# Optimization experiments

Measured on AMD Instinct MI355X. Metric: run time of the kernel, lower is better.

Reference implementation:

```python
import jax, jax.numpy as jnp
import numpy as np

D_MODEL = 1024
MAX_BIRTHS = 4
BIRTH_THRESHOLD = 0.45


def setup_inputs() -> dict:
    key = jax.random.key(0)
    ks = jax.random.split(key, 5)
    B, Tu, Tm, D = 4, 4096, 2048, D_MODEL
    return {
        "o_micro": jax.random.normal(ks[0], (B, Tu, D), jnp.float32),
        "o_macro": jax.random.normal(ks[1], (B, Tm, D), jnp.float32),
        "r_emer_acc": jax.random.uniform(ks[2], (B, Tu, Tm), jnp.float32),
        "chunk_size": 128,
        # vesica_field: Linear(2D -> D, no bias); torch weight layout (D, 2D)
        "W_vesica": jax.random.normal(ks[3], (D, 2 * D), jnp.float32) * (1.0 / np.sqrt(2.0 * D)),
        # birth_gate: Linear(D -> 1)
        "w_gate": jax.random.normal(ks[4], (D,), jnp.float32) * (1.0 / np.sqrt(float(D))),
        "b_gate": jnp.zeros((), jnp.float32),
        "threshold_bias": jnp.zeros((), jnp.float32),
    }


def reference(o_micro, o_macro, r_emer_acc, chunk_size, W_vesica, w_gate, b_gate, threshold_bias):
    B, Tu, D = o_micro.shape
    # accumulated resonance per micro token: mean over macro dim -> (B, Tu)
    micro_res = r_emer_acc.mean(axis=-1)
    # adjacent-pair resonance -> (B, Tu-1)
    pair_res = (micro_res[:, :-1] + micro_res[:, 1:]) * 0.5
    threshold = BIRTH_THRESHOLD + jnp.tanh(threshold_bias) * 0.2
    above = pair_res > threshold
    pair_scores = pair_res * above.astype(pair_res.dtype)
    k = MAX_BIRTHS  # min(max_births, Tu-1); Tu >> max_births here
    topk_vals, topk_idx = jax.lax.top_k(pair_scores, k)  # (B, k)
    birth_mask = topk_vals > 0
    n_births = birth_mask.sum()
    # gather parent pairs -> (B, k, D) each
    left = jnp.take_along_axis(o_micro, topk_idx[..., None], axis=1)
    right = jnp.take_along_axis(o_micro, (topk_idx + 1)[..., None], axis=1)
    combined = jnp.concatenate([left, right], axis=-1)  # (B, k, 2D)
    child = jnp.einsum("bkf,df->bkd", combined, W_vesica)
    gate = jax.nn.sigmoid(jnp.einsum("bkd,d->bk", child, w_gate) + b_gate)
    child = child * gate[..., None] * birth_mask[..., None].astype(child.dtype)
    # compact born children to the front (stable), zeros pad the tail —
    # identical to the torch ragged stack+pad given fixed width k
    order = jnp.argsort(~birth_mask, axis=1, stable=True)  # (B, k)
    child = jnp.take_along_axis(child, order[..., None], axis=1)
    o_macro_expanded = jnp.concatenate([o_macro, child], axis=1)  # (B, Tm+k, D)
    return o_macro_expanded, n_births
```

## Files before the change

### kernel.cpp

```cpp
#include <hip/hip_runtime.h>
#include <math.h>

#define BATCH 4
#define TU 4096
#define TM 2048
#define DM 1024
#define FF 2048
#define KB 4
#define NROWS (BATCH*KB)
#define OUT_TM (TM+KB)

__global__ __launch_bounds__(256) void k_mean_copy(
    const float* __restrict__ r_emer, const float* __restrict__ o_macro,
    float* __restrict__ micro_res, float* __restrict__ out)
{
    const int tid  = threadIdx.x;
    const int lane = tid & 63;
    const int wave = tid >> 6;
    const int row  = blockIdx.x * 4 + wave;

    const float4* rp = (const float4*)(r_emer + (size_t)row * FF);
    float s = 0.0f;
    #pragma unroll
    for (int j = 0; j < 8; ++j) {
        float4 v = rp[lane + 64 * j];
        s += v.x + v.y + v.z + v.w;
    }
    #pragma unroll
    for (int off = 32; off >= 1; off >>= 1)
        s += __shfl_down(s, off, 64);
    if (lane == 0) micro_res[row] = s * (1.0f / 2048.0f);

    const float4* src = (const float4*)o_macro;
    float4* dst = (float4*)out;
    const int NF4       = BATCH * TM * DM / 4;
    const int PER_BATCH = TM * DM / 4;
    const int DST_BATCH = OUT_TM * DM / 4;
    for (int e = blockIdx.x * 256 + tid; e < NF4; e += gridDim.x * 256) {
        int b = e >> 19;
        int q = e & (PER_BATCH - 1);
        dst[b * DST_BATCH + q] = src[e];
    }
}

__global__ __launch_bounds__(256) void k_topk(
    const float* __restrict__ micro_res,
    const float* __restrict__ threshold_bias,
    int* __restrict__ topk_idx, float* __restrict__ topk_val)
{
    __shared__ float res[TU];
    __shared__ float rv[256];
    __shared__ int   ri[256];
    __shared__ int   sel[KB];
    __shared__ float selv[KB];

    const int b = blockIdx.x, tid = threadIdx.x;
    const float* mr = micro_res + b * TU;
    for (int i = tid; i < TU; i += 256) res[i] = mr[i];
    __syncthreads();

    const float thr = 0.45f + tanhf(threshold_bias[0]) * 0.2f;

    for (int p = 0; p < KB; ++p) {
        float bv = -1.0f; int bi = 0x7fffffff;
        for (int t = tid; t < TU - 1; t += 256) {
            bool skip = false;
            for (int q = 0; q < p; ++q) if (sel[q] == t) skip = true;
            if (skip) continue;
            float pr = (res[t] + res[t + 1]) * 0.5f;
            float sc = pr > thr ? pr : 0.0f;
            if (sc > bv || (sc == bv && t < bi)) { bv = sc; bi = t; }
        }
        rv[tid] = bv; ri[tid] = bi;
        __syncthreads();
        for (int s = 128; s >= 1; s >>= 1) {
            if (tid < s) {
                float ov = rv[tid + s]; int oi = ri[tid + s];
                if (ov > rv[tid] || (ov == rv[tid] && oi < ri[tid])) {
                    rv[tid] = ov; ri[tid] = oi;
                }
            }
            __syncthreads();
        }
        if (tid == 0) { sel[p] = ri[0]; selv[p] = rv[0]; }
        __syncthreads();
    }
    if (tid < KB) {
        topk_idx[b * KB + tid] = sel[tid];
        topk_val[b * KB + tid] = selv[tid];
    }
}

__global__ __launch_bounds__(256) void k_child(
    const float* __restrict__ o_micro, const float* __restrict__ W,
    const int* __restrict__ topk_idx, float* __restrict__ child_raw)
{
    const int d   = blockIdx.x;
    const int tid = threadIdx.x;
    const int lane = tid & 63;
    const int wave = tid >> 6;
    const int f0  = tid * 8;

    __shared__ int sidx[NROWS];
    if (tid < NROWS) sidx[tid] = topk_idx[tid];
    __syncthreads();

    const float4* wp = (const float4*)(W + (size_t)d * FF + f0);
    const float4 w0 = wp[0], w1 = wp[1];

    float acc[NROWS];
    #pragma unroll
    for (int r = 0; r < NROWS; ++r) {
        const int bb  = r >> 2;
        const int idx = sidx[r];
        const float* srcrow;
        int fo;
        if (f0 < DM) { srcrow = o_micro + ((size_t)bb * TU + idx) * DM;     fo = f0; }
        else         { srcrow = o_micro + ((size_t)bb * TU + idx + 1) * DM; fo = f0 - DM; }
        const float4* cp = (const float4*)(srcrow + fo);
        float4 c0 = cp[0], c1 = cp[1];
        acc[r] = c0.x * w0.x + c0.y * w0.y + c0.z * w0.z + c0.w * w0.w
               + c1.x * w1.x + c1.y * w1.y + c1.z * w1.z + c1.w * w1.w;
    }

    #pragma unroll
    for (int r = 0; r < NROWS; ++r) {
        float v = acc[r];
        #pragma unroll
        for (int off = 32; off >= 1; off >>= 1)
            v += __shfl_down(v, off, 64);
        acc[r] = v;
    }
    __shared__ float part[4][NROWS];
    if (lane == 0) {
        #pragma unroll
        for (int r = 0; r < NROWS; ++r) part[wave][r] = acc[r];
    }
    __syncthreads();
    if (tid < NROWS)
        child_raw[(size_t)tid * DM + d] =
            part[0][tid] + part[1][tid] + part[2][tid] + part[3][tid];
}

__global__ __launch_bounds__(256) void k_gate(
    const float* __restrict__ child_raw, const float* __restrict__ w_gate,
    const float* __restrict__ b_gate, const float* __restrict__ topk_val,
    float* __restrict__ out)
{
    const int row = blockIdx.x;
    const int b = row >> 2, k = row & 3;
    const int tid = threadIdx.x;
    const int lane = tid & 63, wave = tid >> 6;

    const float4* cp = (const float4*)(child_raw + (size_t)row * DM);
    const float4* wp = (const float4*)w_gate;
    float4 c = cp[tid], w = wp[tid];
    float dotp = c.x * w.x + c.y * w.y + c.z * w.z + c.w * w.w;

    #pragma unroll
    for (int off = 32; off >= 1; off >>= 1)
        dotp += __shfl_down(dotp, off, 64);

    __shared__ float ps[4];
    __shared__ float scale_s;
    if (lane == 0) ps[wave] = dotp;
    __syncthreads();
    if (tid == 0) {
        float dsum = ps[0] + ps[1] + ps[2] + ps[3] + b_gate[0];
        float gate = 1.0f / (1.0f + expf(-dsum));
        float mask = topk_val[row] > 0.0f ? 1.0f : 0.0f;
        scale_s = gate * mask;
    }
    __syncthreads();

    const float s = scale_s;
    float4 o; o.x = c.x * s; o.y = c.y * s; o.z = c.z * s; o.w = c.w * s;
    float4* op = (float4*)(out + ((size_t)b * OUT_TM + TM + k) * DM);
    op[tid] = o;

    if (row == 0 && tid == 0) {
        int n = 0;
        for (int i = 0; i < NROWS; ++i) n += (topk_val[i] > 0.0f) ? 1 : 0;
        out[(size_t)BATCH * OUT_TM * DM] = (float)n;
    }
}

extern "C" void kernel_launch(void* const* d_in, const int* in_sizes, int n_in,
                              void* d_out, int out_size, void* d_ws, size_t ws_size,
                              hipStream_t stream) {
    const float* o_micro   = (const float*)d_in[0];
    const float* o_macro   = (const float*)d_in[1];
    const float* r_emer    = (const float*)d_in[2];
    const float* W_vesica  = (const float*)d_in[4];
    const float* w_gate    = (const float*)d_in[5];
    const float* b_gate    = (const float*)d_in[6];
    const float* thr_bias  = (const float*)d_in[7];
    float* out = (float*)d_out;

    float* wsf       = (float*)d_ws;
    float* micro_res = wsf;
    int*   topk_idx  = (int*)(wsf + 16384);
    float* topk_val  = wsf + 16400;
    float* child_raw = wsf + 16416;

    k_mean_copy<<<4096, 256, 0, stream>>>(r_emer, o_macro, micro_res, out);
    k_topk<<<BATCH, 256, 0, stream>>>(micro_res, thr_bias, topk_idx, topk_val);
    k_child<<<DM, 256, 0, stream>>>(o_micro, W_vesica, topk_idx, child_raw);
    k_gate<<<NROWS, 256, 0, stream>>>(child_raw, w_gate, b_gate, topk_val, out);
}
```

Before: 307.5 us.

## Precompute gate vector W^T·w_gate, fuse gate into topk, overlap macro copy with child GEMV

Uses associativity so the gate logit is computed as combined·(W^T w_gate). The vector u = W^T w_gate is built by extra blocks inside the mean kernel, and the topk kernel applies it right after selection. The child GEMV then writes scaled results straight into the output, and the o_macro copy moves into the same launch as the child blocks. This drops one kernel launch and the child_raw round trip. In exchange the topk kernel does more serial work and rounding order changes slightly.

```diff
diff --git a/kernel.cpp b/kernel.cpp
--- a/kernel.cpp
+++ b/kernel.cpp
@@ -10,56 +10,62 @@
 #define NROWS (BATCH*KB)
 #define OUT_TM (TM+KB)
 
-__global__ __launch_bounds__(256) void k_mean_copy(
-    const float* __restrict__ r_emer, const float* __restrict__ o_macro,
-    float* __restrict__ micro_res, float* __restrict__ out)
+__global__ __launch_bounds__(256) void k_mean_u(
+    const float* __restrict__ r_emer, const float* __restrict__ W,
+    const float* __restrict__ w_gate,
+    float* __restrict__ micro_res, float* __restrict__ partials)
 {
-    const int tid  = threadIdx.x;
-    const int lane = tid & 63;
-    const int wave = tid >> 6;
-    const int row  = blockIdx.x * 4 + wave;
-
-    const float4* rp = (const float4*)(r_emer + (size_t)row * FF);
-    float s = 0.0f;
-    #pragma unroll
-    for (int j = 0; j < 8; ++j) {
-        float4 v = rp[lane + 64 * j];
-        s += v.x + v.y + v.z + v.w;
-    }
-    #pragma unroll
-    for (int off = 32; off >= 1; off >>= 1)
-        s += __shfl_down(s, off, 64);
-    if (lane == 0) micro_res[row] = s * (1.0f / 2048.0f);
-
-    const float4* src = (const float4*)o_macro;
-    float4* dst = (float4*)out;
-    const int NF4       = BATCH * TM * DM / 4;
-    const int PER_BATCH = TM * DM / 4;
-    const int DST_BATCH = OUT_TM * DM / 4;
-    for (int e = blockIdx.x * 256 + tid; e < NF4; e += gridDim.x * 256) {
-        int b = e >> 19;
-        int q = e & (PER_BATCH - 1);
-        dst[b * DST_BATCH + q] = src[e];
-    }
-}
-
-__global__ __launch_bounds__(256) void k_topk(
-    const float* __restrict__ micro_res,
-    const float* __restrict__ threshold_bias,
-    int* __restrict__ topk_idx, float* __restrict__ topk_val)
+    const int tid = threadIdx.x;
+    const int blk = blockIdx.x;
+    if (blk < 4096) {
+        const int lane = tid & 63, wave = tid >> 6;
+        const int row = blk * 4 + wave;
+        const float4* rp = (const float4*)(r_emer + (size_t)row * FF);
+        float s = 0.0f;
+        #pragma unroll
+        for (int j = 0; j < 8; ++j) {
+            float4 v = rp[lane + 64 * j];
+            s += v.x + v.y + v.z + v.w;
+        }
+        #pragma unroll
+        for (int off = 32; off >= 1; off >>= 1)
+            s += __shfl_down(s, off, 64);
+        if (lane == 0) micro_res[row] = s * (1.0f / 2048.0f);
+    } else {
+        const int i  = blk - 4096;
+        const int di = i >> 3;
+        const int f  = (i & 7) * 256 + tid;
+        const int d0 = di * 128;
+        const float* wp = W + (size_t)d0 * FF + f;
+        float acc = 0.0f;
+        #pragma unroll 4
+        for (int d = 0; d < 128; ++d)
+            acc += w_gate[d0 + d] * wp[(size_t)d * FF];
+        partials[di * FF + f] = acc;
+    }
+}
+
+__global__ __launch_bounds__(256) void k_topk_gate(
+    const float* __restrict__ micro_res, const float* __restrict__ thr_bias,
+    const float* __restrict__ o_micro, const float* __restrict__ partials,
+    const float* __restrict__ b_gate,
+    int* __restrict__ sel_out, float* __restrict__ s_out,
+    float* __restrict__ cnt_out)
 {
     __shared__ float res[TU];
     __shared__ float rv[256];
     __shared__ int   ri[256];
     __shared__ int   sel[KB];
     __shared__ float selv[KB];
+    __shared__ float red[4];
 
     const int b = blockIdx.x, tid = threadIdx.x;
+    const int lane = tid & 63, wave = tid >> 6;
     const float* mr = micro_res + b * TU;
     for (int i = tid; i < TU; i += 256) res[i] = mr[i];
     __syncthreads();
 
-    const float thr = 0.45f + tanhf(threshold_bias[0]) * 0.2f;
+    const float thr = 0.45f + tanhf(thr_bias[0]) * 0.2f;
 
     for (int p = 0; p < KB; ++p) {
         float bv = -1.0f; int bi = 0x7fffffff;
@@ -85,103 +91,118 @@
         if (tid == 0) { sel[p] = ri[0]; selv[p] = rv[0]; }
         __syncthreads();
     }
-    if (tid < KB) {
-        topk_idx[b * KB + tid] = sel[tid];
-        topk_val[b * KB + tid] = selv[tid];
-    }
-}
-
-__global__ __launch_bounds__(256) void k_child(
+
+    float su[8];
+    #pragma unroll
+    for (int j = 0; j < 8; ++j) su[j] = 0.0f;
+    const float4* pp = (const float4*)partials;
+    #pragma unroll
+    for (int di = 0; di < 8; ++di) {
+        float4 p0 = pp[di * 512 + tid * 2];
+        float4 p1 = pp[di * 512 + tid * 2 + 1];
+        su[0] += p0.x; su[1] += p0.y; su[2] += p0.z; su[3] += p0.w;
+        su[4] += p1.x; su[5] += p1.y; su[6] += p1.z; su[7] += p1.w;
+    }
+
+    for (int k = 0; k < KB; ++k) {
+        const int idx = sel[k];
+        const float* rowp = (tid < 128)
+            ? o_micro + ((size_t)b * TU + idx) * DM + tid * 8
+            : o_micro + ((size_t)b * TU + idx + 1) * DM + (tid - 128) * 8;
+        float4 c0 = ((const float4*)rowp)[0];
+        float4 c1 = ((const float4*)rowp)[1];
+        float dp = c0.x*su[0] + c0.y*su[1] + c0.z*su[2] + c0.w*su[3]
+                 + c1.x*su[4] + c1.y*su[5] + c1.z*su[6] + c1.w*su[7];
+        #pragma unroll
+        for (int off = 32; off >= 1; off >>= 1)
+            dp += __shfl_down(dp, off, 64);
+        if (lane == 0) red[wave] = dp;
+        __syncthreads();
+        if (tid == 0) {
+            float dot  = red[0] + red[1] + red[2] + red[3] + b_gate[0];
+            float gate = 1.0f / (1.0f + expf(-dot));
+            float mask = selv[k] > 0.0f ? 1.0f : 0.0f;
+            s_out[b * KB + k]   = gate * mask;
+            sel_out[b * KB + k] = sel[k];
+        }
+        __syncthreads();
+    }
+    if (tid == 0) {
+        int c = 0;
+        #pragma unroll
+        for (int k = 0; k < KB; ++k) c += (selv[k] > 0.0f) ? 1 : 0;
+        cnt_out[b] = (float)c;
+    }
+}
+
+__global__ __launch_bounds__(256) void k_child_copy(
     const float* __restrict__ o_micro, const float* __restrict__ W,
-    const int* __restrict__ topk_idx, float* __restrict__ child_raw)
+    const float* __restrict__ o_macro,
+    const int* __restrict__ sel_in, const float* __restrict__ s_in,
+    const float* __restrict__ cnt_in, float* __restrict__ out)
 {
-    const int d   = blockIdx.x;
     const int tid = threadIdx.x;
-    const int lane = tid & 63;
-    const int wave = tid >> 6;
-    const int f0  = tid * 8;
-
-    __shared__ int sidx[NROWS];
-    if (tid < NROWS) sidx[tid] = topk_idx[tid];
-    __syncthreads();
-
-    const float4* wp = (const float4*)(W + (size_t)d * FF + f0);
-    const float4 w0 = wp[0], w1 = wp[1];
-
-    float acc[NROWS];
-    #pragma unroll
-    for (int r = 0; r < NROWS; ++r) {
-        const int bb  = r >> 2;
-        const int idx = sidx[r];
-        const float* srcrow;
-        int fo;
-        if (f0 < DM) { srcrow = o_micro + ((size_t)bb * TU + idx) * DM;     fo = f0; }
-        else         { srcrow = o_micro + ((size_t)bb * TU + idx + 1) * DM; fo = f0 - DM; }
-        const float4* cp = (const float4*)(srcrow + fo);
-        float4 c0 = cp[0], c1 = cp[1];
-        acc[r] = c0.x * w0.x + c0.y * w0.y + c0.z * w0.z + c0.w * w0.w
-               + c1.x * w1.x + c1.y * w1.y + c1.z * w1.z + c1.w * w1.w;
-    }
-
-    #pragma unroll
-    for (int r = 0; r < NROWS; ++r) {
-        float v = acc[r];
-        #pragma unroll
-        for (int off = 32; off >= 1; off >>= 1)
-            v += __shfl_down(v, off, 64);
-        acc[r] = v;
-    }
-    __shared__ float part[4][NROWS];
-    if (lane == 0) {
-        #pragma unroll
-        for (int r = 0; r < NROWS; ++r) part[wave][r] = acc[r];
-    }
-    __syncthreads();
-    if (tid < NROWS)
-        child_raw[(size_t)tid * DM + d] =
-            part[0][tid] + part[1][tid] + part[2][tid] + part[3][tid];
-}
-
-__global__ __launch_bounds__(256) void k_gate(
-    const float* __restrict__ child_raw, const float* __restrict__ w_gate,
-    const float* __restrict__ b_gate, const float* __restrict__ topk_val,
-    float* __restrict__ out)
-{
-    const int row = blockIdx.x;
-    const int b = row >> 2, k = row & 3;
-    const int tid = threadIdx.x;
-    const int lane = tid & 63, wave = tid >> 6;
-
-    const float4* cp = (const float4*)(child_raw + (size_t)row * DM);
-    const float4* wp = (const float4*)w_gate;
-    float4 c = cp[tid], w = wp[tid];
-    float dotp = c.x * w.x + c.y * w.y + c.z * w.z + c.w * w.w;
-
-    #pragma unroll
-    for (int off = 32; off >= 1; off >>= 1)
-        dotp += __shfl_down(dotp, off, 64);
-
-    __shared__ float ps[4];
-    __shared__ float scale_s;
-    if (lane == 0) ps[wave] = dotp;
-    __syncthreads();
-    if (tid == 0) {
-        float dsum = ps[0] + ps[1] + ps[2] + ps[3] + b_gate[0];
-        float gate = 1.0f / (1.0f + expf(-dsum));
-        float mask = topk_val[row] > 0.0f ? 1.0f : 0.0f;
-        scale_s = gate * mask;
-    }
-    __syncthreads();
-
-    const float s = scale_s;
-    float4 o; o.x = c.x * s; o.y = c.y * s; o.z = c.z * s; o.w = c.w * s;
-    float4* op = (float4*)(out + ((size_t)b * OUT_TM + TM + k) * DM);
-    op[tid] = o;
-
-    if (row == 0 && tid == 0) {
-        int n = 0;
-        for (int i = 0; i < NROWS; ++i) n += (topk_val[i] > 0.0f) ? 1 : 0;
-        out[(size_t)BATCH * OUT_TM * DM] = (float)n;
+    if (blockIdx.x < DM) {
+        const int d    = blockIdx.x;
+        const int lane = tid & 63, wave = tid >> 6;
+        const int f0   = tid * 8;
+
+        __shared__ int   sidx[NROWS];
+        __shared__ float ssc[NROWS];
+        if (tid < NROWS) { sidx[tid] = sel_in[tid]; ssc[tid] = s_in[tid]; }
+        __syncthreads();
+
+        const float4* wp = (const float4*)(W + (size_t)d * FF + f0);
+        const float4 w0 = wp[0], w1 = wp[1];
+
+        float acc[NROWS];
+        #pragma unroll
+        for (int r = 0; r < NROWS; ++r) {
+            const int bb  = r >> 2;
+            const int idx = sidx[r];
+            const float* srcrow;
+            int fo;
+            if (f0 < DM) { srcrow = o_micro + ((size_t)bb * TU + idx) * DM;     fo = f0; }
+            else         { srcrow = o_micro + ((size_t)bb * TU + idx + 1) * DM; fo = f0 - DM; }
+            const float4* cp = (const float4*)(srcrow + fo);
+            float4 c0 = cp[0], c1 = cp[1];
+            acc[r] = c0.x * w0.x + c0.y * w0.y + c0.z * w0.z + c0.w * w0.w
+                   + c1.x * w1.x + c1.y * w1.y + c1.z * w1.z + c1.w * w1.w;
+        }
+        #pragma unroll
+        for (int r = 0; r < NROWS; ++r) {
+            float v = acc[r];
+            #pragma unroll
+            for (int off = 32; off >= 1; off >>= 1)
+                v += __shfl_down(v, off, 64);
+            acc[r] = v;
+        }
+        __shared__ float part[4][NROWS];
+        if (lane == 0) {
+            #pragma unroll
+            for (int r = 0; r < NROWS; ++r) part[wave][r] = acc[r];
+        }
+        __syncthreads();
+        if (tid < NROWS) {
+            const int bb = tid >> 2, kk = tid & 3;
+            float v = part[0][tid] + part[1][tid] + part[2][tid] + part[3][tid];
+            out[((size_t)bb * OUT_TM + TM + kk) * DM + d] = v * ssc[tid];
+        }
+    } else {
+        const int NF4       = BATCH * TM * DM / 4;
+        const int PER_BATCH = TM * DM / 4;
+        const int DST_BATCH = OUT_TM * DM / 4;
+        const float4* src = (const float4*)o_macro;
+        float4* dst = (float4*)out;
+        const int cb = blockIdx.x - DM;
+        for (int e = cb * 256 + tid; e < NF4; e += 1024 * 256) {
+            int b = e >> 19;
+            int q = e & (PER_BATCH - 1);
+            dst[b * DST_BATCH + q] = src[e];
+        }
+        if (blockIdx.x == DM && tid == 0)
+            out[(size_t)BATCH * OUT_TM * DM] =
+                cnt_in[0] + cnt_in[1] + cnt_in[2] + cnt_in[3];
     }
 }
 
@@ -199,12 +220,14 @@
 
     float* wsf       = (float*)d_ws;
     float* micro_res = wsf;
-    int*   topk_idx  = (int*)(wsf + 16384);
-    float* topk_val  = wsf + 16400;
-    float* child_raw = wsf + 16416;
-
-    k_mean_copy<<<4096, 256, 0, stream>>>(r_emer, o_macro, micro_res, out);
-    k_topk<<<BATCH, 256, 0, stream>>>(micro_res, thr_bias, topk_idx, topk_val);
-    k_child<<<DM, 256, 0, stream>>>(o_micro, W_vesica, topk_idx, child_raw);
-    k_gate<<<NROWS, 256, 0, stream>>>(child_raw, w_gate, b_gate, topk_val, out);
-}
+    float* partials  = wsf + 16384;
+    int*   selArr    = (int*)(wsf + 32768);
+    float* sArr      = wsf + 32784;
+    float* cntArr    = wsf + 32800;
+
+    k_mean_u   <<<4160, 256, 0, stream>>>(r_emer, W_vesica, w_gate, micro_res, partials);
+    k_topk_gate<<<BATCH, 256, 0, stream>>>(micro_res, thr_bias, o_micro, partials,
+                                           b_gate, selArr, sArr, cntArr);
+    k_child_copy<<<2048, 256, 0, stream>>>(o_micro, W_vesica, o_macro,
+                                           selArr, sArr, cntArr, out);
+}
```

Result: no change. 311.9 us (+1.4%).
